# Optimization experiments

Hardware: AMD Instinct MI355X
Metric: run time of the kernel (lower is better)

## Reference

```python
import jax, jax.numpy as jnp
import numpy as np

N_NODES = 100_000
N_EDGES = 800_000
N_GRAPHS = 5_000
F_NODE = 11
F_EDGE = 4
H1 = 32   # conv1 out channels
H2 = 16   # conv2 out channels


def setup_inputs() -> dict:
    key = jax.random.key(0)
    ks = jax.random.split(key, 20)
    g = lambda i, shape, s=0.1: (jax.random.normal(ks[i], shape, dtype=jnp.float32) * s)
    inp = {
        "x": jax.random.normal(ks[0], (N_NODES, F_NODE), dtype=jnp.float32),
        "edge_index": jax.random.randint(ks[1], (2, N_EDGES), 0, N_NODES, dtype=jnp.int64),
        "edge_attr": jax.random.normal(ks[2], (N_EDGES, F_EDGE), dtype=jnp.float32),
        "batch": jnp.sort(jax.random.randint(ks[3], (N_NODES,), 0, N_GRAPHS, dtype=jnp.int64)),
        # conv1 edge MLP: 4 -> 32 -> 11*32
        "c1_w1": g(4, (F_EDGE, 32)), "c1_b1": jnp.zeros((32,), jnp.float32),
        "c1_w2": g(5, (32, F_NODE * H1)), "c1_b2": jnp.zeros((F_NODE * H1,), jnp.float32),
        "c1_root": g(6, (F_NODE, H1)), "c1_bias": jnp.zeros((H1,), jnp.float32),
        # conv2 edge MLP: 4 -> 32 -> 32*16
        "c2_w1": g(7, (F_EDGE, 32)), "c2_b1": jnp.zeros((32,), jnp.float32),
        "c2_w2": g(8, (32, H1 * H2)), "c2_b2": jnp.zeros((H1 * H2,), jnp.float32),
        "c2_root": g(9, (H1, H2)), "c2_bias": jnp.zeros((H2,), jnp.float32),
        # head
        "fc1_w": g(10, (H2, 32)), "fc1_b": jnp.zeros((32,), jnp.float32),
        "out_w": g(11, (32, 1)), "out_b": jnp.zeros((1,), jnp.float32),
    }
    return inp


def nnconv(x, src, dst, edge_attr, w1, b1, w2, b2, root, bias, c_in, c_out):
    # edge MLP -> per-edge weight matrix [E, c_in, c_out]
    h = jax.nn.relu(edge_attr @ w1 + b1)
    W = (h @ w2 + b2).reshape(-1, c_in, c_out)
    # gather source node features, per-edge matmul, scatter-add to targets
    msg = jnp.einsum("ei,eio->eo", x[src], W)
    agg = jax.ops.segment_sum(msg, dst, num_segments=x.shape[0])
    return agg + x @ root + bias


def reference(x, edge_index, edge_attr, batch,
              c1_w1, c1_b1, c1_w2, c1_b2, c1_root, c1_bias,
              c2_w1, c2_b1, c2_w2, c2_b2, c2_root, c2_bias,
              fc1_w, fc1_b, out_w, out_b):
    src, dst = edge_index[0], edge_index[1]
    h = jax.nn.relu(nnconv(x, src, dst, edge_attr, c1_w1, c1_b1, c1_w2, c1_b2,
                           c1_root, c1_bias, F_NODE, H1))
    h = jax.nn.relu(nnconv(h, src, dst, edge_attr, c2_w1, c2_b1, c2_w2, c2_b2,
                           c2_root, c2_bias, H1, H2))
    pooled = jax.ops.segment_sum(h, batch, num_segments=N_GRAPHS)  # global_add_pool
    h = jax.nn.relu(pooled @ fc1_w + fc1_b)
    return h @ out_w + out_b  # (B, 1)
```

## Files before the change

kernel.cpp:

```cpp
#include <hip/hip_runtime.h>
#include <hip/hip_fp16.h>

#define NNODES 100000
#define NEDGES 800000
#define NGRAPHS 5000
#define FN 11
#define FE 4
#define H1C 32
#define H2C 16

typedef _Float16 half8 __attribute__((ext_vector_type(8)));
typedef float f32x4 __attribute__((ext_vector_type(4)));

__device__ __forceinline__ void pk_atomic_add(_Float16* p, float a, float b) {
  __half2 v = __floats2half2_rn(a, b);
  unsafeAtomicAdd(reinterpret_cast<__half2*>(p), v);
}

__global__ __launch_bounds__(256) void k_prep(const float* __restrict__ c1w2,
    const float* __restrict__ c1b2, _Float16* __restrict__ B1h,
    const float* __restrict__ c2w2, _Float16* __restrict__ B2h) {
  int t = blockIdx.x * 256 + threadIdx.x;
  if (t < 2 * 12 * 64 * 8) {
    int j = t & 7;
    int lane = (t >> 3) & 63;
    int rest = t >> 9;
    int step = rest % 12;
    int ot = rest / 12;
    int q = (lane >> 4) * 8 + j;
    int o = (lane & 15) + ot * 16;
    float v;
    if (step < 11) v = c1w2[q * (FN * H1C) + step * H1C + o];
    else v = (q < FN) ? c1b2[q * H1C + o] : 0.f;
    B1h[t] = (_Float16)v;
  } else {
    int t2 = t - 2 * 12 * 64 * 8;
    if (t2 >= 32 * 64 * 8) return;
    int kk = t2 >> 9;
    int l = (t2 >> 3) & 63;
    int j = t2 & 7;
    int i = (l >> 4) * 8 + j;
    int o = l & 15;
    B2h[t2] = (_Float16)c2w2[(kk * 32 + i) * H2C + o];
  }
}

__global__ __launch_bounds__(256, 3) void k_edge1_mfma(
    const float* __restrict__ x, const int* __restrict__ ei,
    const float* __restrict__ ea, const float* __restrict__ w1,
    const float* __restrict__ b1, const _Float16* __restrict__ B1h,
    _Float16* __restrict__ agg1) {
  __shared__ _Float16 Bl[12288];
  __shared__ _Float16 h_sl[4][256][8];
  __shared__ _Float16 xs_sl[2][256][8];
  __shared__ int s_dst[256];
  int tid = threadIdx.x;
  {
    const int4* s = (const int4*)B1h;
    int4* d = (int4*)Bl;
    #pragma unroll
    for (int q = 0; q < 6; q++) d[q * 256 + tid] = s[q * 256 + tid];
  }
  int e = blockIdx.x * 256 + tid;
  int src = ei[e];
  s_dst[tid] = ei[NEDGES + e];
  float4 a4 = *reinterpret_cast<const float4*>(ea + e * 4);
  float h[32];
  #pragma unroll
  for (int k = 0; k < 32; k++) {
    float v = b1[k] + a4.x * w1[k] + a4.y * w1[32 + k] + a4.z * w1[64 + k] + a4.w * w1[96 + k];
    h[k] = v > 0.f ? v : 0.f;
  }
  #pragma unroll
  for (int s = 0; s < 4; s++) {
    half8 t8;
    #pragma unroll
    for (int j = 0; j < 8; j++) t8[j] = (_Float16)h[s * 8 + j];
    *reinterpret_cast<half8*>(&h_sl[s][tid][0]) = t8;
  }
  float xsv[FN];
  #pragma unroll
  for (int i = 0; i < FN; i++) xsv[i] = x[src * FN + i];
  #pragma unroll
  for (int s = 0; s < 2; s++) {
    half8 t8;
    #pragma unroll
    for (int j = 0; j < 8; j++) {
      int k = s * 8 + j;
      t8[j] = (k < FN) ? (_Float16)xsv[k] : (_Float16)0.f;
    }
    *reinterpret_cast<half8*>(&xs_sl[s][tid][0]) = t8;
  }
  __syncthreads();
  int lane = tid & 63;
  int w = tid >> 6;
  int halfk = lane >> 4;
  int er = lane & 15;
  #pragma unroll 1
  for (int g = 0; g < 4; g++) {
    int eb = w * 64 + g * 16;
    int el = eb + er;
    half8 hs8 = *reinterpret_cast<const half8*>(&h_sl[halfk][el][0]);
    half8 xs8;
    if (halfk < 2) xs8 = *reinterpret_cast<const half8*>(&xs_sl[halfk][el][0]);
    else xs8 = half8{};
    f32x4 acc0 = {0.f, 0.f, 0.f, 0.f};
    f32x4 acc1 = {0.f, 0.f, 0.f, 0.f};
    {
      half8 b0 = *reinterpret_cast<const half8*>(&Bl[11 * 512 + lane * 8]);
      half8 b1f = *reinterpret_cast<const half8*>(&Bl[6144 + 11 * 512 + lane * 8]);
      acc0 = __builtin_amdgcn_mfma_f32_16x16x32_f16(xs8, b0, acc0, 0, 0, 0);
      acc1 = __builtin_amdgcn_mfma_f32_16x16x32_f16(xs8, b1f, acc1, 0, 0, 0);
    }
    #pragma unroll
    for (int i = 0; i < FN; i++) {
      _Float16 xh = xs_sl[i >> 3][el][i & 7];
      half8 xsp;
      #pragma unroll
      for (int j = 0; j < 8; j++) xsp[j] = xh;
      half8 af = xsp * hs8;
      half8 b0 = *reinterpret_cast<const half8*>(&Bl[i * 512 + lane * 8]);
      half8 b1f = *reinterpret_cast<const half8*>(&Bl[6144 + i * 512 + lane * 8]);
      acc0 = __builtin_amdgcn_mfma_f32_16x16x32_f16(af, b0, acc0, 0, 0, 0);
      acc1 = __builtin_amdgcn_mfma_f32_16x16x32_f16(af, b1f, acc1, 0, 0, 0);
    }
    #pragma unroll
    for (int r = 0; r < 4; r++) {
      int d = s_dst[eb + halfk * 4 + r];
      float p0 = __shfl_xor(acc0[r], 1, 64);
      float p1 = __shfl_xor(acc1[r], 1, 64);
      int odd = er & 1;
      int ch = odd ? (16 + er - 1) : er;
      float lo = odd ? p1 : acc0[r];
      float hi = odd ? acc1[r] : p0;
      pk_atomic_add(&agg1[d * H1C + ch], lo, hi);
    }
  }
}

__global__ __launch_bounds__(256) void k_mid(const float* __restrict__ x,
    const _Float16* __restrict__ agg1, const float* __restrict__ root1,
    const float* __restrict__ bias1, const float* __restrict__ root2,
    const float* __restrict__ bias2, _Float16* __restrict__ h1h,
    _Float16* __restrict__ agg2) {
  __shared__ float sbase[16][33];
  int tid = threadIdx.x;
  int t = blockIdx.x * 256 + tid;
  int n = t >> 4, o = t & 15;
  int nl = tid >> 4;
  {
    float b0 = bias1[o], b16 = bias1[o + 16];
    #pragma unroll
    for (int i = 0; i < FN; i++) {
      float xv = x[n * FN + i];
      b0 += xv * root1[i * H1C + o];
      b16 += xv * root1[i * H1C + o + 16];
    }
    sbase[nl][o] = b0;
    sbase[nl][o + 16] = b16;
  }
  __syncthreads();
  float hv[32];
  #pragma unroll
  for (int i = 0; i < 32; i++) {
    float v = (float)agg1[n * H1C + i] + sbase[nl][i];
    hv[i] = v > 0.f ? v : 0.f;
  }
  h1h[n * H1C + o] = (_Float16)hv[o];
  h1h[n * H1C + o + 16] = (_Float16)hv[o + 16];
  float acc = bias2[o];
  #pragma unroll
  for (int i = 0; i < 32; i++) acc += hv[i] * root2[i * H2C + o];
  agg2[n * H2C + o] = (_Float16)acc;
}

__global__ __launch_bounds__(256, 3) void k_edge2_mfma(
    const _Float16* __restrict__ h1h, const int* __restrict__ ei,
    const float* __restrict__ ea, const float* __restrict__ w1,
    const float* __restrict__ b1, const _Float16* __restrict__ B2h,
    _Float16* __restrict__ agg2) {
  __shared__ _Float16 Bl[16384];
  __shared__ _Float16 h_sl2[4][256][8];
  __shared__ int s_src[256];
  __shared__ int s_dst[256];
  int tid = threadIdx.x;
  {
    const int4* s = (const int4*)B2h;
    int4* d = (int4*)Bl;
    #pragma unroll
    for (int q = 0; q < 8; q++) d[q * 256 + tid] = s[q * 256 + tid];
  }
  int e = blockIdx.x * 256 + tid;
  s_src[tid] = ei[e];
  s_dst[tid] = ei[NEDGES + e];
  float4 a4 = *reinterpret_cast<const float4*>(ea + e * 4);
  #pragma unroll
  for (int s = 0; s < 4; s++) {
    half8 t8;
    #pragma unroll
    for (int j = 0; j < 8; j++) {
      int k = s * 8 + j;
      float v = b1[k] + a4.x * w1[k] + a4.y * w1[32 + k] + a4.z * w1[64 + k] + a4.w * w1[96 + k];
      t8[j] = (_Float16)(v > 0.f ? v : 0.f);
    }
    *reinterpret_cast<half8*>(&h_sl2[s][tid][0]) = t8;
  }
  __syncthreads();
  int lane = tid & 63;
  int w = tid >> 6;
  int halfk = lane >> 4;
  int er = lane & 15;
  int sn0 = s_src[w * 64 + er];
  half8 hsb_cur = *reinterpret_cast<const half8*>(h1h + sn0 * H1C + halfk * 8);
  #pragma unroll 1
  for (int g = 0; g < 4; g++) {
    int eb = w * 64 + g * 16;
    int el = eb + er;
    half8 hsb_next = half8{};
    if (g < 3) {
      int sn2 = s_src[eb + 16 + er];
      hsb_next = *reinterpret_cast<const half8*>(h1h + sn2 * H1C + halfk * 8);
    }
    half8 hr0 = *reinterpret_cast<const half8*>(&h_sl2[0][el][0]);
    half8 hr1 = *reinterpret_cast<const half8*>(&h_sl2[1][el][0]);
    half8 hr2 = *reinterpret_cast<const half8*>(&h_sl2[2][el][0]);
    half8 hr3 = *reinterpret_cast<const half8*>(&h_sl2[3][el][0]);
    f32x4 acc = {0.f, 0.f, 0.f, 0.f};
    #pragma unroll
    for (int kk = 0; kk < 32; kk++) {
      _Float16 hv = (kk < 8) ? hr0[kk & 7]
                  : (kk < 16) ? hr1[kk & 7]
                  : (kk < 24) ? hr2[kk & 7]
                  : hr3[kk & 7];
      half8 hsp;
      #pragma unroll
      for (int j = 0; j < 8; j++) hsp[j] = hv;
      half8 af = hsp * hsb_cur;
      half8 bfrag = *reinterpret_cast<const half8*>(&Bl[(kk * 64 + lane) * 8]);
      acc = __builtin_amdgcn_mfma_f32_16x16x32_f16(af, bfrag, acc, 0, 0, 0);
    }
    #pragma unroll
    for (int r2 = 0; r2 < 4; r2 += 2) {
      int d_e = s_dst[eb + halfk * 4 + r2];
      int d_o = s_dst[eb + halfk * 4 + r2 + 1];
      float pe = __shfl_xor(acc[r2], 1, 64);
      float po = __shfl_xor(acc[r2 + 1], 1, 64);
      int odd = er & 1;
      int d = odd ? d_o : d_e;
      int ch = odd ? (er - 1) : er;
      float lo = odd ? po : acc[r2];
      float hi = odd ? acc[r2 + 1] : pe;
      pk_atomic_add(&agg2[d * H2C + ch], lo, hi);
    }
    hsb_cur = hsb_next;
  }
}

__global__ __launch_bounds__(256) void k_poolhead(
    const _Float16* __restrict__ agg2, const int* __restrict__ batch,
    const float* __restrict__ fc1w, const float* __restrict__ fc1b,
    const float* __restrict__ outw, const float* __restrict__ outb,
    float* __restrict__ out) {
  __shared__ float s_p[4][17];
  int tid = threadIdx.x;
  int lane = tid & 63;
  int w = tid >> 6;
  int g = blockIdx.x * 4 + w;
  int lo = 0, hi = NNODES;
  while (lo < hi) { int m = (lo + hi) >> 1; if (batch[m] < g) lo = m + 1; else hi = m; }
  int start = lo;
  hi = NNODES;
  while (lo < hi) { int m = (lo + hi) >> 1; if (batch[m] < g + 1) lo = m + 1; else hi = m; }
  int end = lo;
  int ng = lane >> 4;
  int o = lane & 15;
  float acc = 0.f;
  for (int n = start + ng; n < end; n += 4) {
    float v = (float)agg2[n * H2C + o];
    acc += v > 0.f ? v : 0.f;
  }
  acc += __shfl_xor(acc, 16, 64);
  acc += __shfl_xor(acc, 32, 64);
  if (lane < 16) s_p[w][lane] = acc;
  float vo = 0.f;
  if (lane < 32) {
    float v = fc1b[lane];
    #pragma unroll
    for (int i = 0; i < 16; i++) v += s_p[w][i] * fc1w[i * H1C + lane];
    v = v > 0.f ? v : 0.f;
    vo = v * outw[lane];
  }
  #pragma unroll
  for (int ofs = 32; ofs >= 1; ofs >>= 1) vo += __shfl_xor(vo, ofs, 64);
  if (lane == 0) out[g] = vo + outb[0];
}

extern "C" void kernel_launch(void* const* d_in, const int* in_sizes, int n_in,
                              void* d_out, int out_size, void* d_ws, size_t ws_size,
                              hipStream_t stream) {
  const float* x      = (const float*)d_in[0];
  const int*   ei     = (const int*)d_in[1];
  const float* ea     = (const float*)d_in[2];
  const int*   batch  = (const int*)d_in[3];
  const float* c1w1   = (const float*)d_in[4];
  const float* c1b1   = (const float*)d_in[5];
  const float* c1w2   = (const float*)d_in[6];
  const float* c1b2   = (const float*)d_in[7];
  const float* c1root = (const float*)d_in[8];
  const float* c1bias = (const float*)d_in[9];
  const float* c2w1   = (const float*)d_in[10];
  const float* c2b1   = (const float*)d_in[11];
  const float* c2w2   = (const float*)d_in[12];
  const float* c2b2   = (const float*)d_in[13];
  const float* c2root = (const float*)d_in[14];
  const float* c2bias = (const float*)d_in[15];
  const float* fc1w   = (const float*)d_in[16];
  const float* fc1b   = (const float*)d_in[17];
  const float* outw   = (const float*)d_in[18];
  const float* outb   = (const float*)d_in[19];
  float* out = (float*)d_out;

  _Float16*  agg1   = (_Float16*)d_ws;
  _Float16*  h1h    = agg1 + NNODES * H1C;
  _Float16*  agg2   = h1h + NNODES * H1C;
  _Float16*  B2h    = agg2 + NNODES * H2C;
  _Float16*  B1h    = B2h + 32 * 64 * 8;

  hipMemsetAsync(agg1, 0, (size_t)NNODES * H1C * sizeof(_Float16), stream);

  k_prep<<<112, 256, 0, stream>>>(c1w2, c1b2, B1h, c2w2, B2h);
  k_edge1_mfma<<<NEDGES / 256, 256, 0, stream>>>(x, ei, ea, c1w1, c1b1, B1h, agg1);
  k_mid<<<NNODES * H2C / 256, 256, 0, stream>>>(x, agg1, c1root, c1bias,
                                                c2root, c2bias, h1h, agg2);
  k_edge2_mfma<<<NEDGES / 256, 256, 0, stream>>>(h1h, ei, ea, c2w1, c2b1, B2h, agg2);
  k_poolhead<<<NGRAPHS / 4, 256, 0, stream>>>(agg2, batch, fc1w, fc1b, outw, outb, out);
}
```

Before: 141.0 us.

## Fold agg1 zeroing into prep kernel and split edge2 MFMA accumulator chain

Removes the separate hipMemsetAsync for agg1 and instead zeroes it inside k_prep, which now launches enough blocks to cover the buffer. This drops one launch. In k_edge2_mfma the 32-step MFMA accumulation is split across two independent accumulators that are summed at the end, to break the serial dependency between consecutive MFMAs. The cost is extra registers and a slightly different fp32 summation order.

```diff
diff --git a/kernel.cpp b/kernel.cpp
--- a/kernel.cpp
+++ b/kernel.cpp
@@ -19,8 +19,13 @@
 
 __global__ __launch_bounds__(256) void k_prep(const float* __restrict__ c1w2,
     const float* __restrict__ c1b2, _Float16* __restrict__ B1h,
-    const float* __restrict__ c2w2, _Float16* __restrict__ B2h) {
+    const float* __restrict__ c2w2, _Float16* __restrict__ B2h,
+    _Float16* __restrict__ agg1) {
   int t = blockIdx.x * 256 + threadIdx.x;
+  if (t < NNODES * H1C / 8) {
+    int4 z = {0, 0, 0, 0};
+    reinterpret_cast<int4*>(agg1)[t] = z;
+  }
   if (t < 2 * 12 * 64 * 8) {
     int j = t & 7;
     int lane = (t >> 3) & 63;
@@ -33,9 +38,8 @@
     if (step < 11) v = c1w2[q * (FN * H1C) + step * H1C + o];
     else v = (q < FN) ? c1b2[q * H1C + o] : 0.f;
     B1h[t] = (_Float16)v;
-  } else {
+  } else if (t < 2 * 12 * 64 * 8 + 32 * 64 * 8) {
     int t2 = t - 2 * 12 * 64 * 8;
-    if (t2 >= 32 * 64 * 8) return;
     int kk = t2 >> 9;
     int l = (t2 >> 3) & 63;
     int j = t2 & 7;
@@ -225,20 +229,39 @@
     half8 hr1 = *reinterpret_cast<const half8*>(&h_sl2[1][el][0]);
     half8 hr2 = *reinterpret_cast<const half8*>(&h_sl2[2][el][0]);
     half8 hr3 = *reinterpret_cast<const half8*>(&h_sl2[3][el][0]);
-    f32x4 acc = {0.f, 0.f, 0.f, 0.f};
-    #pragma unroll
-    for (int kk = 0; kk < 32; kk++) {
-      _Float16 hv = (kk < 8) ? hr0[kk & 7]
-                  : (kk < 16) ? hr1[kk & 7]
-                  : (kk < 24) ? hr2[kk & 7]
-                  : hr3[kk & 7];
-      half8 hsp;
-      #pragma unroll
-      for (int j = 0; j < 8; j++) hsp[j] = hv;
-      half8 af = hsp * hsb_cur;
-      half8 bfrag = *reinterpret_cast<const half8*>(&Bl[(kk * 64 + lane) * 8]);
-      acc = __builtin_amdgcn_mfma_f32_16x16x32_f16(af, bfrag, acc, 0, 0, 0);
-    }
+    f32x4 accA = {0.f, 0.f, 0.f, 0.f};
+    f32x4 accB = {0.f, 0.f, 0.f, 0.f};
+    #pragma unroll
+    for (int kk = 0; kk < 32; kk += 2) {
+      {
+        _Float16 hv = (kk < 8) ? hr0[kk & 7]
+                    : (kk < 16) ? hr1[kk & 7]
+                    : (kk < 24) ? hr2[kk & 7]
+                    : hr3[kk & 7];
+        half8 hsp;
+        #pragma unroll
+        for (int j = 0; j < 8; j++) hsp[j] = hv;
+        half8 af = hsp * hsb_cur;
+        half8 bfrag = *reinterpret_cast<const half8*>(&Bl[(kk * 64 + lane) * 8]);
+        accA = __builtin_amdgcn_mfma_f32_16x16x32_f16(af, bfrag, accA, 0, 0, 0);
+      }
+      {
+        int k2 = kk + 1;
+        _Float16 hv = (k2 < 8) ? hr0[k2 & 7]
+                    : (k2 < 16) ? hr1[k2 & 7]
+                    : (k2 < 24) ? hr2[k2 & 7]
+                    : hr3[k2 & 7];
+        half8 hsp;
+        #pragma unroll
+        for (int j = 0; j < 8; j++) hsp[j] = hv;
+        half8 af = hsp * hsb_cur;
+        half8 bfrag = *reinterpret_cast<const half8*>(&Bl[(k2 * 64 + lane) * 8]);
+        accB = __builtin_amdgcn_mfma_f32_16x16x32_f16(af, bfrag, accB, 0, 0, 0);
+      }
+    }
+    f32x4 acc;
+    #pragma unroll
+    for (int r = 0; r < 4; r++) acc[r] = accA[r] + accB[r];
     #pragma unroll
     for (int r2 = 0; r2 < 4; r2 += 2) {
       int d_e = s_dst[eb + halfk * 4 + r2];
@@ -326,9 +349,8 @@
   _Float16*  B2h    = agg2 + NNODES * H2C;
   _Float16*  B1h    = B2h + 32 * 64 * 8;
 
-  hipMemsetAsync(agg1, 0, (size_t)NNODES * H1C * sizeof(_Float16), stream);
-
-  k_prep<<<112, 256, 0, stream>>>(c1w2, c1b2, B1h, c2w2, B2h);
+  k_prep<<<(NNODES * H1C / 8 + 255) / 256, 256, 0, stream>>>(
+      c1w2, c1b2, B1h, c2w2, B2h, agg1);
   k_edge1_mfma<<<NEDGES / 256, 256, 0, stream>>>(x, ei, ea, c1w1, c1b1, B1h, agg1);
   k_mid<<<NNODES * H2C / 256, 256, 0, stream>>>(x, agg1, c1root, c1bias,
                                                 c2root, c2bias, h1h, agg2);
```

Result: no change. 138.5 us (-1.8%).
